# Kernel optimization log

Measured on AMD Instinct MI355X. Metric: run time of the kernel, lower is better.

Reference implementation:

```python
import jax, jax.numpy as jnp
import numpy as np

EMB = 1024
HEAD = 64

def setup_inputs() -> dict:
    key = jax.random.key(0)
    k1, k2, k3, k4, k5 = jax.random.split(key, 5)
    x = jax.random.normal(k1, (4, 4096, EMB), dtype=jnp.float32)
    # qkv linear: weight [3*HEAD, EMB] torch-style -> store as [EMB, 3*HEAD]
    W_qkv = jax.random.normal(k2, (EMB, 3 * HEAD), dtype=jnp.float32) * (1.0 / np.sqrt(EMB))
    b_qkv = jax.random.normal(k3, (3 * HEAD,), dtype=jnp.float32) * 0.01
    W_out = jax.random.normal(k4, (HEAD, EMB), dtype=jnp.float32) * (1.0 / np.sqrt(HEAD))
    b_out = jax.random.normal(k5, (EMB,), dtype=jnp.float32) * 0.01
    return {"x": x, "W_qkv": W_qkv, "b_qkv": b_qkv, "W_out": W_out, "b_out": b_out}

def reference(x, W_qkv, b_qkv, W_out, b_out):
    qkv = jnp.einsum('bse,ed->bsd', x, W_qkv) + b_qkv            # [B,S,3H]
    q, k, v = jnp.split(qkv, 3, axis=-1)                          # each [B,S,H]
    scale = 1.0 / jnp.sqrt(jnp.asarray(q.shape[-1], q.dtype))
    scores = jnp.einsum('bqh,bkh->bqk', q, k) * scale             # [B,S,S]
    attn = jax.nn.softmax(scores, axis=-1)
    ctx = jnp.einsum('bqk,bkh->bqh', attn, v)                     # [B,S,H]
    return jnp.einsum('bqh,he->bqe', ctx, W_out) + b_out          # [B,S,E]
```

## Files before the change

### kernel.cpp

```cpp
#include <hip/hip_runtime.h>
#include <hip/hip_bf16.h>


#define LD 72

typedef __attribute__((ext_vector_type(8))) short short8;
typedef __attribute__((ext_vector_type(4))) short short4v;
typedef __attribute__((ext_vector_type(4))) float floatx4;

#define MFMA(a, b, c) __builtin_amdgcn_mfma_f32_16x16x32_bf16((a), (b), (c), 0, 0, 0)

__device__ __forceinline__ unsigned short f2bf(float f) {
  union { float f; unsigned u; } c; c.f = f;
  unsigned u = c.u + 0x7fffu + ((c.u >> 16) & 1u);
  return (unsigned short)(u >> 16);
}
__device__ __forceinline__ float asf(unsigned u) {
  union { unsigned u; float f; } c; c.u = u; return c.f;
}

__global__ __launch_bounds__(256) void prep_kernel(
    const float* __restrict__ Wqkv, const float* __restrict__ Wout,
    unsigned short* __restrict__ WtQkv, unsigned short* __restrict__ WtOut) {
  int idx = blockIdx.x * 256 + threadIdx.x;
  if (idx < 192 * 1024) {
    int n = idx >> 10, k = idx & 1023;
    WtQkv[idx] = f2bf(Wqkv[k * 192 + n]);
  } else if (idx < 192 * 1024 + 1024 * 64) {
    int j = idx - 192 * 1024;
    int e = j >> 6, d = j & 63;
    WtOut[j] = f2bf(Wout[d * 1024 + e]);
  }
}

__global__ __launch_bounds__(256, 2) void qkv_kernel(
    const float* __restrict__ x, const unsigned short* __restrict__ WtQkv,
    const float* __restrict__ bqkv,
    unsigned short* __restrict__ Qg, unsigned short* __restrict__ Kg,
    unsigned short* __restrict__ Vtg) {
  __shared__ __align__(16) unsigned short XS[2][32 * LD];
  __shared__ __align__(16) unsigned short WS[2][192 * LD];

  const int tid = threadIdx.x;
  const int wave = tid >> 6, lane = tid & 63, quad = lane >> 4, l16 = lane & 15;
  const int row0 = blockIdx.x * 32;
  const int colbase = wave * 48;

  floatx4 acc[2][3];
#pragma unroll
  for (int rt = 0; rt < 2; rt++)
#pragma unroll
    for (int t = 0; t < 3; t++) acc[rt][t] = (floatx4)(0.0f);

  const int xr = tid >> 3, xj = tid & 7;
  const float* gx = x + (size_t)(row0 + xr) * 1024 + xj * 8;
  const unsigned short* gw = WtQkv + (size_t)xr * 1024 + xj * 8;

  {
    float4 xa = *(const float4*)(gx);
    float4 xb = *(const float4*)(gx + 4);
    uint4 wv[6];
#pragma unroll
    for (int i = 0; i < 6; i++) wv[i] = *(const uint4*)(gw + i * 32768);
    short8 xc;
    xc[0] = (short)f2bf(xa.x); xc[1] = (short)f2bf(xa.y);
    xc[2] = (short)f2bf(xa.z); xc[3] = (short)f2bf(xa.w);
    xc[4] = (short)f2bf(xb.x); xc[5] = (short)f2bf(xb.y);
    xc[6] = (short)f2bf(xb.z); xc[7] = (short)f2bf(xb.w);
    *(short8*)(&XS[0][xr * LD + xj * 8]) = xc;
#pragma unroll
    for (int i = 0; i < 6; i++)
      *(uint4*)(&WS[0][(xr + 32 * i) * LD + xj * 8]) = wv[i];
  }
  __syncthreads();

  for (int kc = 0; kc < 16; kc++) {
    const int buf = kc & 1;
    float4 nxa, nxb;
    uint4 nwv[6];
    if (kc < 15) {
      const float* gxn = gx + (kc + 1) * 64;
      nxa = *(const float4*)(gxn);
      nxb = *(const float4*)(gxn + 4);
      const unsigned short* gwn = gw + (kc + 1) * 64;
#pragma unroll
      for (int i = 0; i < 6; i++) nwv[i] = *(const uint4*)(gwn + i * 32768);
    }
    short8 a0 = *(const short8*)(&XS[buf][l16 * LD + quad * 8]);
    short8 a0h = *(const short8*)(&XS[buf][l16 * LD + 32 + quad * 8]);
    short8 a1 = *(const short8*)(&XS[buf][(16 + l16) * LD + quad * 8]);
    short8 a1h = *(const short8*)(&XS[buf][(16 + l16) * LD + 32 + quad * 8]);
#pragma unroll
    for (int t = 0; t < 3; t++) {
      short8 b0 = *(const short8*)(&WS[buf][(colbase + t * 16 + l16) * LD + quad * 8]);
      short8 b1 = *(const short8*)(&WS[buf][(colbase + t * 16 + l16) * LD + 32 + quad * 8]);
      acc[0][t] = MFMA(a0, b0, acc[0][t]);
      acc[0][t] = MFMA(a0h, b1, acc[0][t]);
      acc[1][t] = MFMA(a1, b0, acc[1][t]);
      acc[1][t] = MFMA(a1h, b1, acc[1][t]);
    }
    if (kc < 15) {
      short8 xc;
      xc[0] = (short)f2bf(nxa.x); xc[1] = (short)f2bf(nxa.y);
      xc[2] = (short)f2bf(nxa.z); xc[3] = (short)f2bf(nxa.w);
      xc[4] = (short)f2bf(nxb.x); xc[5] = (short)f2bf(nxb.y);
      xc[6] = (short)f2bf(nxb.z); xc[7] = (short)f2bf(nxb.w);
      *(short8*)(&XS[buf ^ 1][xr * LD + xj * 8]) = xc;
#pragma unroll
      for (int i = 0; i < 6; i++)
        *(uint4*)(&WS[buf ^ 1][(xr + 32 * i) * LD + xj * 8]) = nwv[i];
    }
    __syncthreads();
  }

  unsigned short* eQ = &XS[0][0];
  unsigned short* eK = &XS[1][0];
  unsigned short* eV = &WS[0][0];
  const int b = row0 >> 12, srow = row0 & 4095;
#pragma unroll
  for (int rt = 0; rt < 2; rt++)
#pragma unroll
    for (int t = 0; t < 3; t++) {
      int col = colbase + t * 16 + l16;
      float bias = bqkv[col];
      int sec = col >> 6, d = col & 63;
#pragma unroll
      for (int r = 0; r < 4; r++) {
        int lrow = rt * 16 + quad * 4 + r;
        float v = acc[rt][t][r] + bias;
        if (sec == 0)      eQ[lrow * LD + d] = f2bf(v * 0.125f);
        else if (sec == 1) eK[lrow * LD + d] = f2bf(v);
        else               eV[d * 40 + lrow] = f2bf(v);
      }
    }
  __syncthreads();
  {
    int r = tid >> 3, sg = tid & 7;
    *(uint4*)(Qg + (size_t)(row0 + r) * 64 + sg * 8) = *(const uint4*)(&eQ[r * LD + sg * 8]);
    *(uint4*)(Kg + (size_t)(row0 + r) * 64 + sg * 8) = *(const uint4*)(&eK[r * LD + sg * 8]);
    int tile = tid >> 7, rem = tid & 127, d = rem >> 1, half = rem & 1;
    *(uint4*)(Vtg + (((size_t)b * 256 + (srow >> 4) + tile) * 64 + d) * 16 + half * 8)
        = *(const uint4*)(&eV[d * 40 + tile * 16 + half * 8]);
  }
}

__global__ __launch_bounds__(256, 4) void attn_kernel(
    const unsigned short* __restrict__ Qg, const unsigned short* __restrict__ Kg,
    const unsigned short* __restrict__ Vtg,
    unsigned short* __restrict__ Opart, float* __restrict__ Lpart) {
  __shared__ __align__(16) unsigned short Ks[64 * LD];
  __shared__ __align__(16) unsigned short Vs[64 * LD];
  __shared__ __align__(16) unsigned short QP[64 * LD];

  const int tid = threadIdx.x;
  const int wave = tid >> 6, lane = tid & 63, quad = lane >> 4, l16 = lane & 15;
  const int bid = blockIdx.x;
  const int combo = bid & 15, qt = bid >> 4;
  const int b = combo >> 2, split = combo & 3;
  const int q0 = qt * 64, key0 = split * 1024;

  {
    int r = tid >> 2, seg = tid & 3;
    const uint4* s = (const uint4*)(Qg + ((size_t)b * 4096 + q0 + r) * 64 + seg * 16);
    *(uint4*)(&QP[r * LD + seg * 16])     = s[0];
    *(uint4*)(&QP[r * LD + seg * 16 + 8]) = s[1];
  }
  short8 aq0 = *(const short8*)(&QP[(wave * 16 + l16) * LD + quad * 8]);
  short8 aq1 = *(const short8*)(&QP[(wave * 16 + l16) * LD + 32 + quad * 8]);

  floatx4 o[4];
  float lsum[4];
#pragma unroll
  for (int t = 0; t < 4; t++) o[t] = (floatx4)(0.0f);
#pragma unroll
  for (int r = 0; r < 4; r++) lsum[r] = 0.0f;

  const int kr = tid >> 2, kseg = tid & 3;
  const unsigned short* Kbase = Kg + ((size_t)b * 4096 + key0) * 64;
  const unsigned short* Vt0 = Vtg + ((size_t)b * 256 + (key0 >> 4)) * 1024;

  uint4 pk0, pk1, pv0, pv1;
  pk0 = *(const uint4*)(Kbase + (size_t)kr * 64 + kseg * 16);
  pk1 = *(const uint4*)(Kbase + (size_t)kr * 64 + kseg * 16 + 8);
  pv0 = *(const uint4*)(Vt0 + ((size_t)kseg * 64 + kr) * 16);
  pv1 = *(const uint4*)(Vt0 + ((size_t)kseg * 64 + kr) * 16 + 8);

  unsigned short* Pw = &QP[wave * 16 * LD];

  for (int kc = 0; kc < 16; kc++) {
    __syncthreads();
    *(uint4*)(&Ks[kr * LD + kseg * 16])     = pk0;
    *(uint4*)(&Ks[kr * LD + kseg * 16 + 8]) = pk1;
    *(uint4*)(&Vs[kr * LD + kseg * 16])     = pv0;
    *(uint4*)(&Vs[kr * LD + kseg * 16 + 8]) = pv1;
    __syncthreads();
    if (kc < 15) {
      int nk = (kc + 1) * 64;
      int tl = (kc + 1) * 4 + kseg;
      pk0 = *(const uint4*)(Kbase + (size_t)(nk + kr) * 64 + kseg * 16);
      pk1 = *(const uint4*)(Kbase + (size_t)(nk + kr) * 64 + kseg * 16 + 8);
      pv0 = *(const uint4*)(Vt0 + ((size_t)tl * 64 + kr) * 16);
      pv1 = *(const uint4*)(Vt0 + ((size_t)tl * 64 + kr) * 16 + 8);
    }

    floatx4 sc[4];
#pragma unroll
    for (int t = 0; t < 4; t++) sc[t] = (floatx4)(0.0f);
#pragma unroll
    for (int t = 0; t < 4; t++) {
      short8 b0 = *(const short8*)(&Ks[(t * 16 + l16) * LD + quad * 8]);
      short8 b1 = *(const short8*)(&Ks[(t * 16 + l16) * LD + 32 + quad * 8]);
      sc[t] = MFMA(aq0, b0, sc[t]);
      sc[t] = MFMA(aq1, b1, sc[t]);
    }

#pragma unroll
    for (int r = 0; r < 4; r++) {
#pragma unroll
      for (int t = 0; t < 4; t++) {
        float pv = __expf(sc[t][r]);
        lsum[r] += pv;
        Pw[(quad * 4 + r) * LD + t * 16 + l16] = f2bf(pv);
      }
    }
    short8 ap0 = *(const short8*)(&Pw[l16 * LD + quad * 8]);
    short8 ap1 = *(const short8*)(&Pw[l16 * LD + 32 + quad * 8]);
#pragma unroll
    for (int t = 0; t < 4; t++) {
      short8 b0 = *(const short8*)(&Vs[(t * 16 + l16) * LD + quad * 8]);
      short8 b1 = *(const short8*)(&Vs[(t * 16 + l16) * LD + 32 + quad * 8]);
      o[t] = MFMA(ap0, b0, o[t]);
      o[t] = MFMA(ap1, b1, o[t]);
    }
  }

#pragma unroll
  for (int r = 0; r < 4; r++) {
#pragma unroll
    for (int off = 1; off < 16; off <<= 1) lsum[r] += __shfl_xor(lsum[r], off, 64);
  }

  unsigned short* Ob = Opart + ((size_t)bid * 64 + wave * 16) * 64;
#pragma unroll
  for (int t = 0; t < 4; t++)
#pragma unroll
    for (int r = 0; r < 4; r++)
      Ob[(quad * 4 + r) * 64 + t * 16 + l16] = f2bf(o[t][r]);
  if (l16 == 0) {
#pragma unroll
    for (int r = 0; r < 4; r++)
      Lpart[bid * 64 + wave * 16 + quad * 4 + r] = lsum[r];
  }
}

__global__ __launch_bounds__(256, 4) void combine_kernel(
    const unsigned short* __restrict__ Opart, const float* __restrict__ Lpart,
    const unsigned short* __restrict__ WtOut, const float* __restrict__ bout,
    float* __restrict__ out) {
  __shared__ __align__(16) unsigned short Cs[4][16 * LD];
  __shared__ __align__(16) unsigned short Wl[128 * LD];

  const int tid = threadIdx.x;
  const int wave = tid >> 6, lane = tid & 63, quad = lane >> 4, l16 = lane & 15;
  const int cid = blockIdx.x;
  const int eq = cid & 3, qt = (cid >> 2) & 63, b = cid >> 8;
  const int e0 = eq * 256;

  const int q = lane >> 2, d0 = (lane & 3) * 16;
  float accv[16];
#pragma unroll
  for (int i = 0; i < 16; i++) accv[i] = 0.0f;
  float lq = 0.0f;
#pragma unroll
  for (int s = 0; s < 4; s++) {
    int pid = qt * 16 + b * 4 + s;
    const unsigned short* src = Opart + ((size_t)pid * 64 + wave * 16 + q) * 64 + d0;
    uint4 h0 = *(const uint4*)src;
    uint4 h1 = *(const uint4*)(src + 8);
    const unsigned* hw = (const unsigned*)&h0;
#pragma unroll
    for (int i = 0; i < 4; i++) {
      accv[2 * i]     += asf(hw[i] << 16);
      accv[2 * i + 1] += asf(hw[i] & 0xFFFF0000u);
    }
    const unsigned* hw1 = (const unsigned*)&h1;
#pragma unroll
    for (int i = 0; i < 4; i++) {
      accv[8 + 2 * i]     += asf(hw1[i] << 16);
      accv[8 + 2 * i + 1] += asf(hw1[i] & 0xFFFF0000u);
    }
    lq += Lpart[pid * 64 + wave * 16 + q];
  }
  float inv = 1.0f / lq;
  short8 c0, c1;
#pragma unroll
  for (int i = 0; i < 8; i++) {
    c0[i] = (short)f2bf(accv[i] * inv);
    c1[i] = (short)f2bf(accv[8 + i] * inv);
  }
  *(short8*)(&Cs[wave][q * LD + d0])     = c0;
  *(short8*)(&Cs[wave][q * LD + d0 + 8]) = c1;
  short8 ao0 = *(const short8*)(&Cs[wave][l16 * LD + quad * 8]);
  short8 ao1 = *(const short8*)(&Cs[wave][l16 * LD + 32 + quad * 8]);

  const size_t orow0 = (size_t)b * 4096 + qt * 64 + wave * 16;
#pragma unroll 1
  for (int ec = 0; ec < 2; ec++) {
    int ebase = e0 + ec * 128;
    __syncthreads();
    {
      int er = tid >> 1, half = tid & 1;
      const uint4* s = (const uint4*)(WtOut + (size_t)(ebase + er) * 64 + half * 32);
      uint4 w0 = s[0], w1 = s[1], w2 = s[2], w3 = s[3];
      *(uint4*)(&Wl[er * LD + half * 32])      = w0;
      *(uint4*)(&Wl[er * LD + half * 32 + 8])  = w1;
      *(uint4*)(&Wl[er * LD + half * 32 + 16]) = w2;
      *(uint4*)(&Wl[er * LD + half * 32 + 24]) = w3;
    }
    __syncthreads();
    floatx4 a2[8];
#pragma unroll
    for (int t = 0; t < 8; t++) a2[t] = (floatx4)(0.0f);
#pragma unroll
    for (int t = 0; t < 8; t++) {
      short8 b0 = *(const short8*)(&Wl[(t * 16 + l16) * LD + quad * 8]);
      short8 b1 = *(const short8*)(&Wl[(t * 16 + l16) * LD + 32 + quad * 8]);
      a2[t] = MFMA(ao0, b0, a2[t]);
      a2[t] = MFMA(ao1, b1, a2[t]);
    }
#pragma unroll
    for (int t = 0; t < 8; t++) {
      int e = ebase + t * 16 + l16;
      float bo = bout[e];
#pragma unroll
      for (int r = 0; r < 4; r++)
        out[(orow0 + quad * 4 + r) * 1024 + e] = a2[t][r] + bo;
    }
  }
}

extern "C" void kernel_launch(void* const* d_in, const int* in_sizes, int n_in,
                              void* d_out, int out_size, void* d_ws, size_t ws_size,
                              hipStream_t stream) {
  const float* x    = (const float*)d_in[0];
  const float* Wqkv = (const float*)d_in[1];
  const float* bqkv = (const float*)d_in[2];
  const float* Wout = (const float*)d_in[3];
  const float* bout = (const float*)d_in[4];
  float* out = (float*)d_out;

  unsigned short* ws = (unsigned short*)d_ws;
  unsigned short* Qg    = ws;
  unsigned short* Kg    = Qg + 1048576;
  unsigned short* Vtg   = Kg + 1048576;
  unsigned short* WtQkv = Vtg + 1048576;
  unsigned short* WtOut = WtQkv + 196608;
  unsigned short* Opart = WtOut + 65536;
  float*          Lpart = (float*)(Opart + 4194304);

  prep_kernel<<<1024, 256, 0, stream>>>(Wqkv, Wout, WtQkv, WtOut);
  qkv_kernel<<<512, 256, 0, stream>>>(x, WtQkv, bqkv, Qg, Kg, Vtg);
  attn_kernel<<<1024, 256, 0, stream>>>(Qg, Kg, Vtg, Opart, Lpart);
  combine_kernel<<<1024, 256, 0, stream>>>(Opart, Lpart, WtOut, bout, out);
}
```

Before: 184.4 us.

## Permute key order in P and V layout to pack P stores with hardware bf16 convert

Stores the softmax probabilities for four key tiles as one packed 8-byte LDS write per row, using the v_cvt_pk_bf16_f32 instruction instead of scalar f2bf conversions and 2-byte stores. To keep the P·V product correct under the permuted key ordering (key t*16+l16 now sits at column l16*4+t), the QKV epilogue writes V transposed in a matching interleaved 64-key-block layout, and the attention kernel's V loads are updated to match. This cuts LDS store instructions and conversion ALU work in the inner loop. The cost is a more scattered 4-byte global write pattern for V in the projection kernel.

```diff
diff --git a/kernel.cpp b/kernel.cpp
--- a/kernel.cpp
+++ b/kernel.cpp
@@ -138,9 +138,18 @@
     int r = tid >> 3, sg = tid & 7;
     *(uint4*)(Qg + (size_t)(row0 + r) * 64 + sg * 8) = *(const uint4*)(&eQ[r * LD + sg * 8]);
     *(uint4*)(Kg + (size_t)(row0 + r) * 64 + sg * 8) = *(const uint4*)(&eK[r * LD + sg * 8]);
-    int tile = tid >> 7, rem = tid & 127, d = rem >> 1, half = rem & 1;
-    *(uint4*)(Vtg + (((size_t)b * 256 + (srow >> 4) + tile) * 64 + d) * 16 + half * 8)
-        = *(const uint4*)(&eV[d * 40 + tile * 16 + half * 8]);
+  }
+  {
+    const int g = srow >> 6, k0 = (srow & 63) >> 4;
+    int d = tid >> 2, i4 = tid & 3;
+    unsigned short* vb = Vtg + (((size_t)b * 64 + g) * 64 + d) * 64 + k0;
+#pragma unroll
+    for (int ii = 0; ii < 4; ii++) {
+      int idx = i4 * 4 + ii;
+      unsigned lo = eV[d * 40 + idx];
+      unsigned hi = eV[d * 40 + 16 + idx];
+      *(unsigned*)(vb + idx * 4) = lo | (hi << 16);
+    }
   }
 }
 
@@ -177,13 +186,13 @@
 
   const int kr = tid >> 2, kseg = tid & 3;
   const unsigned short* Kbase = Kg + ((size_t)b * 4096 + key0) * 64;
-  const unsigned short* Vt0 = Vtg + ((size_t)b * 256 + (key0 >> 4)) * 1024;
+  const unsigned short* Vt0 = Vtg + ((size_t)b * 64 + (key0 >> 6)) * 4096;
 
   uint4 pk0, pk1, pv0, pv1;
   pk0 = *(const uint4*)(Kbase + (size_t)kr * 64 + kseg * 16);
   pk1 = *(const uint4*)(Kbase + (size_t)kr * 64 + kseg * 16 + 8);
-  pv0 = *(const uint4*)(Vt0 + ((size_t)kseg * 64 + kr) * 16);
-  pv1 = *(const uint4*)(Vt0 + ((size_t)kseg * 64 + kr) * 16 + 8);
+  pv0 = *(const uint4*)(Vt0 + (size_t)kr * 64 + kseg * 16);
+  pv1 = *(const uint4*)(Vt0 + (size_t)kr * 64 + kseg * 16 + 8);
 
   unsigned short* Pw = &QP[wave * 16 * LD];
 
@@ -196,11 +205,10 @@
     __syncthreads();
     if (kc < 15) {
       int nk = (kc + 1) * 64;
-      int tl = (kc + 1) * 4 + kseg;
       pk0 = *(const uint4*)(Kbase + (size_t)(nk + kr) * 64 + kseg * 16);
       pk1 = *(const uint4*)(Kbase + (size_t)(nk + kr) * 64 + kseg * 16 + 8);
-      pv0 = *(const uint4*)(Vt0 + ((size_t)tl * 64 + kr) * 16);
-      pv1 = *(const uint4*)(Vt0 + ((size_t)tl * 64 + kr) * 16 + 8);
+      pv0 = *(const uint4*)(Vt0 + (size_t)(kc + 1) * 4096 + kr * 64 + kseg * 16);
+      pv1 = *(const uint4*)(Vt0 + (size_t)(kc + 1) * 4096 + kr * 64 + kseg * 16 + 8);
     }
 
     floatx4 sc[4];
@@ -216,12 +224,16 @@
 
 #pragma unroll
     for (int r = 0; r < 4; r++) {
-#pragma unroll
-      for (int t = 0; t < 4; t++) {
-        float pv = __expf(sc[t][r]);
-        lsum[r] += pv;
-        Pw[(quad * 4 + r) * LD + t * 16 + l16] = f2bf(pv);
-      }
+      float e0 = __expf(sc[0][r]);
+      float e1 = __expf(sc[1][r]);
+      float e2 = __expf(sc[2][r]);
+      float e3 = __expf(sc[3][r]);
+      lsum[r] += (e0 + e1) + (e2 + e3);
+      unsigned w0, w1;
+      asm("v_cvt_pk_bf16_f32 %0, %1, %2" : "=v"(w0) : "v"(e0), "v"(e1));
+      asm("v_cvt_pk_bf16_f32 %0, %1, %2" : "=v"(w1) : "v"(e2), "v"(e3));
+      uint2 pw; pw.x = w0; pw.y = w1;
+      *(uint2*)(&Pw[(quad * 4 + r) * LD + l16 * 4]) = pw;
     }
     short8 ap0 = *(const short8*)(&Pw[l16 * LD + quad * 8]);
     short8 ap1 = *(const short8*)(&Pw[l16 * LD + 32 + quad * 8]);
```

Result: no change. 180.9 us, median of 3 (-1.9%).
